# Performance work log

Hardware: AMD Instinct MI355X
Metric: run time of the kernel (lower is better)

## Reference

```python
import jax, jax.numpy as jnp
import numpy as np

B, T, D = 4, 2048, 1024
H, DH = 16, 64
GH = H * DH  # == D here
SCALE = DH ** -0.5
LN_EPS = 1e-5


def setup_inputs() -> dict:
    key = jax.random.key(0)
    ks = jax.random.split(key, 8)
    x = jax.random.normal(ks[0], (B, T, D), dtype=jnp.float32)
    attn_mask = jax.random.uniform(ks[1], (T, T), dtype=jnp.float32)
    # LayerNorm params
    gamma = jnp.ones((D,), jnp.float32)
    beta = jnp.zeros((D,), jnp.float32)
    # projection weights, stored (in, out) so y = x @ W
    Wq = jax.random.normal(ks[2], (D, GH), jnp.float32) * (D ** -0.5)
    Wk = jax.random.normal(ks[3], (D, GH), jnp.float32) * (D ** -0.5)
    Wv = jax.random.normal(ks[4], (D, GH), jnp.float32) * (D ** -0.5)
    Wo = jax.random.normal(ks[5], (GH, D), jnp.float32) * (GH ** -0.5)
    bo = jnp.zeros((D,), jnp.float32)
    return {"x": x, "attn_mask": attn_mask, "gamma": gamma, "beta": beta,
            "Wq": Wq, "Wk": Wk, "Wv": Wv, "Wo": Wo, "bo": bo}


def reference(x, attn_mask, gamma, beta, Wq, Wk, Wv, Wo, bo):
    # LayerNorm over last dim
    mu = jnp.mean(x, axis=-1, keepdims=True)
    var = jnp.mean((x - mu) ** 2, axis=-1, keepdims=True)
    xn = (x - mu) * jax.lax.rsqrt(var + LN_EPS) * gamma + beta
    # QKV projections (bias=False), reshape to [B, H, T, DH]
    split = lambda y: y.reshape(B, T, H, DH).transpose(0, 2, 1, 3)
    q = split(xn @ Wq)
    k = split(xn @ Wk)
    v = split(xn @ Wv)
    # scores scaled then MULTIPLICATIVELY masked (post-scale)
    scores = jnp.einsum('bhqd,bhkd->bhqk', q, k) * SCALE
    scores = scores * attn_mask  # broadcast [T,T] over [B,H,T,T]
    probs = jax.nn.softmax(scores, axis=-1)  # dropout p=0 -> identity
    av = jnp.einsum('bhqk,bhkd->bhqd', probs, v)
    av = av.transpose(0, 2, 1, 3).reshape(B, T, GH)
    return av @ Wo + bo
```

## Files before the change

### kernel.cpp

```cpp
#include <hip/hip_runtime.h>

typedef unsigned short u16;
typedef unsigned int u32;
typedef __bf16 bf16x8 __attribute__((ext_vector_type(8)));
typedef float f32x4 __attribute__((ext_vector_type(4)));

#define AS1 __attribute__((address_space(1)))
#define AS3 __attribute__((address_space(3)))

#define SWZB(x) ((x) ^ ((((x) >> 7) & 7) << 4))

__device__ __forceinline__ float bf2f(u16 u) {
    union { u32 i; float f; } v; v.i = ((u32)u) << 16; return v.f;
}
__device__ __forceinline__ u16 f2bf(float f) {
    union { float f; u32 i; } v; v.f = f;
    u32 i = v.i;
    u32 r = (i + 0x7fffu + ((i >> 16) & 1u)) >> 16;
    return (u16)r;
}
__device__ __forceinline__ float blo(u32 u) {
    union { u32 i; float f; } v; v.i = u << 16; return v.f;
}
__device__ __forceinline__ float bhi(u32 u) {
    union { u32 i; float f; } v; v.i = u & 0xFFFF0000u; return v.f;
}
__device__ __forceinline__ u32 cvtpk_bf16(float lo, float hi) {
    u32 r;
    asm("v_cvt_pk_bf16_f32 %0, %1, %2" : "=v"(r) : "v"(lo), "v"(hi));
    return r;
}
__device__ __forceinline__ float fexp2(float x) {
    float r;
    asm("v_exp_f32 %0, %1" : "=v"(r) : "v"(x));
    return r;
}
__device__ __forceinline__ void gload_lds16(const u16* src, u16* dst) {
    __builtin_amdgcn_global_load_lds((const AS1 void*)src, (AS3 void*)dst, 16, 0, 0);
}

__global__ __launch_bounds__(256) void transposeW(const float* __restrict__ Wq,
                                                  const float* __restrict__ Wk,
                                                  const float* __restrict__ Wv,
                                                  const float* __restrict__ Wo,
                                                  u16* __restrict__ WT,
                                                  u16* __restrict__ WoT) {
    __shared__ u16 t[64][65];
    int z = blockIdx.z;
    const float* in = (z == 0) ? Wq : (z == 1) ? Wk : (z == 2) ? Wv : Wo;
    u16* out = (z < 3) ? WT + (size_t)z * 1024 * 1024 : WoT;
    float scale = (z == 0) ? 0.18033688f : 1.0f;
    int c = threadIdx.x & 63, r0 = threadIdx.x >> 6;
    int ib = blockIdx.y * 64, jb = blockIdx.x * 64;
    #pragma unroll
    for (int r = r0; r < 64; r += 4)
        t[r][c] = f2bf(in[(size_t)(ib + r) * 1024 + jb + c] * scale);
    __syncthreads();
    #pragma unroll
    for (int r = r0; r < 64; r += 4) out[(size_t)(jb + r) * 1024 + ib + c] = t[c][r];
}

__global__ __launch_bounds__(256) void maskprep(const float* __restrict__ in,
                                                u16* __restrict__ out) {
    int i = blockIdx.x * 256 + threadIdx.x;
    float4 v = *(const float4*)&in[(size_t)i * 4];
    ushort4 o;
    o.x = f2bf(v.x); o.y = f2bf(v.y); o.z = f2bf(v.z); o.w = f2bf(v.w);
    *(ushort4*)&out[(size_t)i * 4] = o;
}

__global__ __launch_bounds__(256) void ln_kernel(const float* __restrict__ x,
                                                 const float* __restrict__ g,
                                                 const float* __restrict__ bb,
                                                 u16* __restrict__ xn) {
    int row = blockIdx.x;
    int tid = threadIdx.x;
    const float* xr = x + (size_t)row * 1024;
    float4 v = *(const float4*)&xr[tid * 4];
    float f0 = v.x, f1 = v.y, f2 = v.z, f3 = v.w;
    float s = f0 + f1 + f2 + f3;
    float sq = f0 * f0 + f1 * f1 + f2 * f2 + f3 * f3;
    #pragma unroll
    for (int m = 1; m < 64; m <<= 1) { s += __shfl_xor(s, m, 64); sq += __shfl_xor(sq, m, 64); }
    __shared__ float red[8];
    int wid = tid >> 6, lane = tid & 63;
    if (lane == 0) { red[wid] = s; red[4 + wid] = sq; }
    __syncthreads();
    s = red[0] + red[1] + red[2] + red[3];
    sq = red[4] + red[5] + red[6] + red[7];
    float mu = s * (1.f / 1024.f);
    float var = sq * (1.f / 1024.f) - mu * mu;
    float rs = rsqrtf(var + 1e-5f);
    float4 gv = *(const float4*)&g[tid * 4];
    float4 bv = *(const float4*)&bb[tid * 4];
    ushort4 o;
    o.x = f2bf((f0 - mu) * rs * gv.x + bv.x);
    o.y = f2bf((f1 - mu) * rs * gv.y + bv.y);
    o.z = f2bf((f2 - mu) * rs * gv.z + bv.z);
    o.w = f2bf((f3 - mu) * rs * gv.w + bv.w);
    *(ushort4*)&xn[(size_t)row * 1024 + tid * 4] = o;
}

__global__ __launch_bounds__(256) void gemm_bt(const u16* __restrict__ A,
                                               const u16* __restrict__ BT,
                                               u16* __restrict__ C16,
                                               float* __restrict__ C32,
                                               const float* __restrict__ bias,
                                               int K, int ldc, int ext, int nbx,
                                               u16* __restrict__ vTout) {
    __shared__ __align__(16) u16 lA[128 * 32];
    __shared__ __align__(16) u16 lB[128 * 32];
    int bid = blockIdx.x;
    int xcd = bid & 7, loc = bid >> 3;
    int npx = nbx >> 3;
    int n0 = (xcd * npx + loc % npx) * 128;
    int m0 = (loc / npx) * 128;
    int tid = threadIdx.x, lane = tid & 63, wid = tid >> 6;
    int wr = wid >> 1, wc = wid & 1;
    int l4 = lane >> 4, l15 = lane & 15;

    f32x4 acc[4][4] = {};
    int NT = K >> 5;

    auto stage = [&](int kt) {
        int k0 = kt << 5;
        #pragma unroll
        for (int i = 0; i < 2; ++i) {
            int j = wid * 2 + i;
            int row = j * 16 + (lane >> 2);
            int ch = (lane & 3) * 8;
            gload_lds16(A + (size_t)(m0 + row) * K + k0 + ch, &lA[j * 512]);
            gload_lds16(BT + (size_t)(n0 + row) * K + k0 + ch, &lB[j * 512]);
        }
    };
    stage(0);
    for (int kt = 0; kt < NT; ++kt) {
        __syncthreads();
        bf16x8 af[4], bfr[4];
        #pragma unroll
        for (int i = 0; i < 4; ++i) {
            af[i]  = *(const bf16x8*)&lA[(wr * 64 + i * 16 + l15) * 32 + l4 * 8];
            bfr[i] = *(const bf16x8*)&lB[(wc * 64 + i * 16 + l15) * 32 + l4 * 8];
        }
        __syncthreads();
        if (kt + 1 < NT) stage(kt + 1);
        #pragma unroll
        for (int i = 0; i < 4; ++i)
            #pragma unroll
            for (int j = 0; j < 4; ++j)
                acc[i][j] = __builtin_amdgcn_mfma_f32_16x16x32_bf16(af[i], bfr[j], acc[i][j], 0, 0, 0);
    }
    bool vblk = (vTout != nullptr) && (n0 >= 2048);
    #pragma unroll
    for (int j = 0; j < 4; ++j) {
        int col = n0 + wc * 64 + j * 16 + l15;
        if (vblk) {
            int hd = col - 2048;
            #pragma unroll
            for (int i = 0; i < 4; ++i) {
                int trow = m0 + wr * 64 + i * 16 + l4 * 4;
                int bidx = trow >> 11, t = trow & 2047;
                ushort4 pk;
                pk.x = f2bf(acc[i][j][0]);
                pk.y = f2bf(acc[i][j][1]);
                pk.z = f2bf(acc[i][j][2]);
                pk.w = f2bf(acc[i][j][3]);
                *(ushort4*)&vTout[(size_t)(bidx * 1024 + hd) * 2048 + t] = pk;
            }
        } else {
            float bv = ext ? bias[col] : 0.f;
            #pragma unroll
            for (int i = 0; i < 4; ++i) {
                #pragma unroll
                for (int r = 0; r < 4; ++r) {
                    int row = m0 + wr * 64 + i * 16 + l4 * 4 + r;
                    float val = acc[i][j][r] + bv;
                    if (ext) C32[(size_t)row * ldc + col] = val;
                    else     C16[(size_t)row * ldc + col] = f2bf(val);
                }
            }
        }
    }
}

__global__ __launch_bounds__(256) void attn_kernel(const u16* __restrict__ qkv,
                                                   const u16* __restrict__ vT,
                                                   const u16* __restrict__ maskb,
                                                   u16* __restrict__ av) {
    __shared__ __align__(16) u16 lK[2][64 * 64];
    __shared__ __align__(16) u16 lV[2][64 * 64];
    int qt = blockIdx.x, bh = blockIdx.y;
    int b = bh >> 4, h = bh & 15;
    int tid = threadIdx.x, lane = tid & 63, wid = tid >> 6;
    int l4 = lane >> 4, l15 = lane & 15;
    int qw = qt * 128 + wid * 32;

    const u16* qb0 = qkv + (size_t)(b * 2048 + qw + l15) * 2048 + h * 64;
    const u16* qb1 = qb0 + (size_t)16 * 2048;
    bf16x8 qf00 = *(const bf16x8*)&qb0[l4 * 8];
    bf16x8 qf01 = *(const bf16x8*)&qb0[32 + l4 * 8];
    bf16x8 qf10 = *(const bf16x8*)&qb1[l4 * 8];
    bf16x8 qf11 = *(const bf16x8*)&qb1[32 + l4 * 8];
    const u16* mrow0 = maskb + (size_t)(qw + l15) * 2048 + 8 * l4;
    const u16* mrow1 = mrow0 + (size_t)16 * 2048;

    f32x4 o0[4] = {}, o1[4] = {};
    float lsum0 = 0.f, lsum1 = 0.f;

    int c0 = tid, c1 = 256 + tid;
    auto pmap = [](int g) {
        return (g & 32) + 4 * ((g >> 3) & 3) + (g & 3) + ((g & 4) << 2);
    };
    int kd0 = SWZB(pmap(c0 >> 3) * 128 + (c0 & 7) * 16);
    int kd1 = SWZB(pmap(c1 >> 3) * 128 + (c1 & 7) * 16);
    int vd0 = SWZB((c0 >> 3) * 128 + (c0 & 7) * 16);
    int vd1 = SWZB((c1 >> 3) * 128 + (c1 & 7) * 16);
    const u16* ksrc0 = qkv + (size_t)(b * 2048 + (c0 >> 3)) * 2048 + 1024 + h * 64 + (c0 & 7) * 8;
    const u16* ksrc1 = qkv + (size_t)(b * 2048 + (c1 >> 3)) * 2048 + 1024 + h * 64 + (c1 & 7) * 8;
    const u16* vsrc0 = vT + (size_t)(bh * 64 + (c0 >> 3)) * 2048 + (c0 & 7) * 8;
    const u16* vsrc1 = vT + (size_t)(bh * 64 + (c1 >> 3)) * 2048 + (c1 & 7) * 8;

    auto loadKV = [&](int t, bf16x8& K0, bf16x8& K1, bf16x8& V0, bf16x8& V1) {
        size_t ko = (size_t)t * (64 * 2048);
        int vo = t * 64;
        K0 = *(const bf16x8*)(ksrc0 + ko);
        K1 = *(const bf16x8*)(ksrc1 + ko);
        V0 = *(const bf16x8*)(vsrc0 + vo);
        V1 = *(const bf16x8*)(vsrc1 + vo);
    };

    union PU { u32 u[4]; bf16x8 v; };

    auto body = [&](int t, int pbuf,
                    bf16x8& nK0, bf16x8& nK1, bf16x8& nV0, bf16x8& nV1,
                    bf16x8& fK0, bf16x8& fK1, bf16x8& fV0, bf16x8& fV1) {
        int k0 = t * 64;
        uint4 mua0 = *(const uint4*)(mrow0 + k0);
        uint4 mub0 = *(const uint4*)(mrow0 + k0 + 32);
        uint4 mua1 = *(const uint4*)(mrow1 + k0);
        uint4 mub1 = *(const uint4*)(mrow1 + k0 + 32);
        f32x4 mm0[4], mm1[4];
        mm0[0] = f32x4{blo(mua0.x), bhi(mua0.x), blo(mua0.y), bhi(mua0.y)};
        mm0[1] = f32x4{blo(mua0.z), bhi(mua0.z), blo(mua0.w), bhi(mua0.w)};
        mm0[2] = f32x4{blo(mub0.x), bhi(mub0.x), blo(mub0.y), bhi(mub0.y)};
        mm0[3] = f32x4{blo(mub0.z), bhi(mub0.z), blo(mub0.w), bhi(mub0.w)};
        mm1[0] = f32x4{blo(mua1.x), bhi(mua1.x), blo(mua1.y), bhi(mua1.y)};
        mm1[1] = f32x4{blo(mua1.z), bhi(mua1.z), blo(mua1.w), bhi(mua1.w)};
        mm1[2] = f32x4{blo(mub1.x), bhi(mub1.x), blo(mub1.y), bhi(mub1.y)};
        mm1[3] = f32x4{blo(mub1.z), bhi(mub1.z), blo(mub1.w), bhi(mub1.w)};
        const char* Kb = (const char*)lK[pbuf];
        f32x4 s0[4] = {}, s1[4] = {};
        __builtin_amdgcn_s_setprio(1);
        #pragma unroll
        for (int fj = 0; fj < 4; ++fj) {
            bf16x8 kf0 = *(const bf16x8*)(Kb + SWZB((fj * 16 + l15) * 128 + l4 * 16));
            bf16x8 kf1 = *(const bf16x8*)(Kb + SWZB((fj * 16 + l15) * 128 + 64 + l4 * 16));
            s0[fj] = __builtin_amdgcn_mfma_f32_16x16x32_bf16(kf0, qf00, s0[fj], 0, 0, 0);
            s0[fj] = __builtin_amdgcn_mfma_f32_16x16x32_bf16(kf1, qf01, s0[fj], 0, 0, 0);
            s1[fj] = __builtin_amdgcn_mfma_f32_16x16x32_bf16(kf0, qf10, s1[fj], 0, 0, 0);
            s1[fj] = __builtin_amdgcn_mfma_f32_16x16x32_bf16(kf1, qf11, s1[fj], 0, 0, 0);
        }
        __builtin_amdgcn_s_setprio(0);
        PU pa0[2], pa1[2];
        #pragma unroll
        for (int fj = 0; fj < 4; ++fj) {
            float p0 = fexp2(s0[fj][0] * mm0[fj][0]);
            float p1 = fexp2(s0[fj][1] * mm0[fj][1]);
            float p2 = fexp2(s0[fj][2] * mm0[fj][2]);
            float p3 = fexp2(s0[fj][3] * mm0[fj][3]);
            lsum0 += (p0 + p1) + (p2 + p3);
            int ks = fj >> 1, hf = (fj & 1) * 2;
            pa0[ks].u[hf]     = cvtpk_bf16(p0, p1);
            pa0[ks].u[hf + 1] = cvtpk_bf16(p2, p3);
        }
        #pragma unroll
        for (int fj = 0; fj < 4; ++fj) {
            float p0 = fexp2(s1[fj][0] * mm1[fj][0]);
            float p1 = fexp2(s1[fj][1] * mm1[fj][1]);
            float p2 = fexp2(s1[fj][2] * mm1[fj][2]);
            float p3 = fexp2(s1[fj][3] * mm1[fj][3]);
            lsum1 += (p0 + p1) + (p2 + p3);
            int ks = fj >> 1, hf = (fj & 1) * 2;
            pa1[ks].u[hf]     = cvtpk_bf16(p0, p1);
            pa1[ks].u[hf + 1] = cvtpk_bf16(p2, p3);
        }
        if (t + 1 < 32) {
            char* Kn = (char*)lK[pbuf ^ 1];
            char* Vn = (char*)lV[pbuf ^ 1];
            *(bf16x8*)(Kn + kd0) = nK0;
            *(bf16x8*)(Kn + kd1) = nK1;
            *(bf16x8*)(Vn + vd0) = nV0;
            *(bf16x8*)(Vn + vd1) = nV1;
        }
        if (t + 2 < 32) loadKV(t + 2, fK0, fK1, fV0, fV1);
        const char* Vb = (const char*)lV[pbuf];
        __builtin_amdgcn_s_setprio(1);
        #pragma unroll
        for (int ks = 0; ks < 2; ++ks) {
            #pragma unroll
            for (int fj = 0; fj < 4; ++fj) {
                bf16x8 vf = *(const bf16x8*)(Vb + SWZB((fj * 16 + l15) * 128 + ks * 64 + l4 * 16));
                o0[fj] = __builtin_amdgcn_mfma_f32_16x16x32_bf16(pa0[ks].v, vf, o0[fj], 0, 0, 0);
                o1[fj] = __builtin_amdgcn_mfma_f32_16x16x32_bf16(pa1[ks].v, vf, o1[fj], 0, 0, 0);
            }
        }
        __builtin_amdgcn_s_setprio(0);
        __syncthreads();
    };

    bf16x8 ka0, ka1, va0, va1, kb0, kb1, vb0, vb1;
    loadKV(0, ka0, ka1, va0, va1);
    *(bf16x8*)((char*)lK[0] + kd0) = ka0;
    *(bf16x8*)((char*)lK[0] + kd1) = ka1;
    *(bf16x8*)((char*)lV[0] + vd0) = va0;
    *(bf16x8*)((char*)lV[0] + vd1) = va1;
    loadKV(1, kb0, kb1, vb0, vb1);
    __syncthreads();
    for (int t = 0; t < 32; t += 2) {
        body(t,     0, kb0, kb1, vb0, vb1, ka0, ka1, va0, va1);
        body(t + 1, 1, ka0, ka1, va0, va1, kb0, kb1, vb0, vb1);
    }

    lsum0 += __shfl_xor(lsum0, 16, 64);
    lsum0 += __shfl_xor(lsum0, 32, 64);
    lsum1 += __shfl_xor(lsum1, 16, 64);
    lsum1 += __shfl_xor(lsum1, 32, 64);
    float den0[4], den1[4];
    #pragma unroll
    for (int r = 0; r < 4; ++r) {
        den0[r] = __shfl(lsum0, l4 * 4 + r, 64);
        den1[r] = __shfl(lsum1, l4 * 4 + r, 64);
    }
    #pragma unroll
    for (int fj = 0; fj < 4; ++fj) {
        #pragma unroll
        for (int r = 0; r < 4; ++r) {
            int col = h * 64 + fj * 16 + l15;
            av[(size_t)(b * 2048 + qw + l4 * 4 + r) * 1024 + col]      = f2bf(o0[fj][r] / den0[r]);
            av[(size_t)(b * 2048 + qw + 16 + l4 * 4 + r) * 1024 + col] = f2bf(o1[fj][r] / den1[r]);
        }
    }
}

extern "C" void kernel_launch(void* const* d_in, const int* in_sizes, int n_in,
                              void* d_out, int out_size, void* d_ws, size_t ws_size,
                              hipStream_t stream) {
    (void)in_sizes; (void)n_in; (void)out_size; (void)ws_size;
    const float* x     = (const float*)d_in[0];
    const float* mask  = (const float*)d_in[1];
    const float* gamma = (const float*)d_in[2];
    const float* beta  = (const float*)d_in[3];
    const float* Wq    = (const float*)d_in[4];
    const float* Wk    = (const float*)d_in[5];
    const float* Wv    = (const float*)d_in[6];
    const float* Wo    = (const float*)d_in[7];
    const float* bo    = (const float*)d_in[8];

    char* ws = (char*)d_ws;
    u16* xn    = (u16*)(ws);
    u16* WT    = (u16*)(ws + 16777216);
    u16* WoT   = (u16*)(ws + 23068672);
    u16* qkvb  = (u16*)(ws + 25165824);
    u16* vT    = (u16*)(ws + 58720256);
    u16* maskb = (u16*)(ws + 75497472);
    u16* av = xn;

    dim3 tb(256);
    transposeW<<<dim3(16, 16, 4), tb, 0, stream>>>(Wq, Wk, Wv, Wo, WT, WoT);
    maskprep<<<4096, tb, 0, stream>>>(mask, maskb);
    ln_kernel<<<8192, tb, 0, stream>>>(x, gamma, beta, xn);
    gemm_bt<<<24 * 64, tb, 0, stream>>>(xn, WT, qkvb, nullptr, nullptr, 1024, 2048, 0, 24, vT);
    attn_kernel<<<dim3(16, 64), tb, 0, stream>>>(qkvb, vT, maskb, av);
    gemm_bt<<<8 * 64, tb, 0, stream>>>(av, WoT, nullptr, (float*)d_out, bo, 1024, 1024, 1, 8, nullptr);
}
```

Before: 243.0 us.

## Stage K/V tiles with direct global-to-LDS loads instead of register staging

Replaces register-staged K/V prefetch (global load into VGPRs, then ds_write into swizzled LDS) with direct global-to-LDS loads. To keep the swizzled and permuted LDS layout, the source addresses are inverted from each thread's linear LDS slot. Prefetch depth drops from two tiles ahead to one, and the body is a plain loop. This frees registers and LDS-write instructions, but exposes more load latency and relies on gload_lds16 being defined and completing before the existing barrier.

```diff
diff --git a/kernel.cpp b/kernel.cpp
--- a/kernel.cpp
+++ b/kernel.cpp
@@ -208,32 +208,34 @@
     float lsum0 = 0.f, lsum1 = 0.f;
 
     int c0 = tid, c1 = 256 + tid;
-    auto pmap = [](int g) {
-        return (g & 32) + 4 * ((g >> 3) & 3) + (g & 3) + ((g & 4) << 2);
+    auto pinv = [](int p) {
+        return (p & 35) | ((p & 8) << 1) | ((p & 4) << 1) | ((p & 16) >> 2);
     };
-    int kd0 = SWZB(pmap(c0 >> 3) * 128 + (c0 & 7) * 16);
-    int kd1 = SWZB(pmap(c1 >> 3) * 128 + (c1 & 7) * 16);
-    int vd0 = SWZB((c0 >> 3) * 128 + (c0 & 7) * 16);
-    int vd1 = SWZB((c1 >> 3) * 128 + (c1 & 7) * 16);
-    const u16* ksrc0 = qkv + (size_t)(b * 2048 + (c0 >> 3)) * 2048 + 1024 + h * 64 + (c0 & 7) * 8;
-    const u16* ksrc1 = qkv + (size_t)(b * 2048 + (c1 >> 3)) * 2048 + 1024 + h * 64 + (c1 & 7) * 8;
-    const u16* vsrc0 = vT + (size_t)(bh * 64 + (c0 >> 3)) * 2048 + (c0 & 7) * 8;
-    const u16* vsrc1 = vT + (size_t)(bh * 64 + (c1 >> 3)) * 2048 + (c1 & 7) * 8;
-
-    auto loadKV = [&](int t, bf16x8& K0, bf16x8& K1, bf16x8& V0, bf16x8& V1) {
+    int u0 = SWZB(c0 * 16), u1 = SWZB(c1 * 16);
+    int kr0 = pinv(u0 >> 7), kr1 = pinv(u1 >> 7);
+    int vr0 = u0 >> 7,       vr1 = u1 >> 7;
+    int ch0 = (u0 >> 4) & 7, ch1 = (u1 >> 4) & 7;
+    const u16* kap0 = qkv + (size_t)(b * 2048 + kr0) * 2048 + 1024 + h * 64 + ch0 * 8;
+    const u16* kap1 = qkv + (size_t)(b * 2048 + kr1) * 2048 + 1024 + h * 64 + ch1 * 8;
+    const u16* vap0 = vT + (size_t)(bh * 64 + vr0) * 2048 + ch0 * 8;
+    const u16* vap1 = vT + (size_t)(bh * 64 + vr1) * 2048 + ch1 * 8;
+
+    auto stage = [&](int t, int buf) {
         size_t ko = (size_t)t * (64 * 2048);
         int vo = t * 64;
-        K0 = *(const bf16x8*)(ksrc0 + ko);
-        K1 = *(const bf16x8*)(ksrc1 + ko);
-        V0 = *(const bf16x8*)(vsrc0 + vo);
-        V1 = *(const bf16x8*)(vsrc1 + vo);
+        gload_lds16(kap0 + ko, &lK[buf][wid * 512]);
+        gload_lds16(kap1 + ko, &lK[buf][2048 + wid * 512]);
+        gload_lds16(vap0 + vo, &lV[buf][wid * 512]);
+        gload_lds16(vap1 + vo, &lV[buf][2048 + wid * 512]);
     };
 
     union PU { u32 u[4]; bf16x8 v; };
 
-    auto body = [&](int t, int pbuf,
-                    bf16x8& nK0, bf16x8& nK1, bf16x8& nV0, bf16x8& nV1,
-                    bf16x8& fK0, bf16x8& fK1, bf16x8& fV0, bf16x8& fV1) {
+    stage(0, 0);
+    __syncthreads();
+    for (int t = 0; t < 32; ++t) {
+        int pbuf = t & 1;
+        if (t + 1 < 32) stage(t + 1, pbuf ^ 1);
         int k0 = t * 64;
         uint4 mua0 = *(const uint4*)(mrow0 + k0);
         uint4 mub0 = *(const uint4*)(mrow0 + k0 + 32);
@@ -284,15 +286,6 @@
             pa1[ks].u[hf]     = cvtpk_bf16(p0, p1);
             pa1[ks].u[hf + 1] = cvtpk_bf16(p2, p3);
         }
-        if (t + 1 < 32) {
-            char* Kn = (char*)lK[pbuf ^ 1];
-            char* Vn = (char*)lV[pbuf ^ 1];
-            *(bf16x8*)(Kn + kd0) = nK0;
-            *(bf16x8*)(Kn + kd1) = nK1;
-            *(bf16x8*)(Vn + vd0) = nV0;
-            *(bf16x8*)(Vn + vd1) = nV1;
-        }
-        if (t + 2 < 32) loadKV(t + 2, fK0, fK1, fV0, fV1);
         const char* Vb = (const char*)lV[pbuf];
         __builtin_amdgcn_s_setprio(1);
         #pragma unroll
@@ -306,19 +299,6 @@
         }
         __builtin_amdgcn_s_setprio(0);
         __syncthreads();
-    };
-
-    bf16x8 ka0, ka1, va0, va1, kb0, kb1, vb0, vb1;
-    loadKV(0, ka0, ka1, va0, va1);
-    *(bf16x8*)((char*)lK[0] + kd0) = ka0;
-    *(bf16x8*)((char*)lK[0] + kd1) = ka1;
-    *(bf16x8*)((char*)lV[0] + vd0) = va0;
-    *(bf16x8*)((char*)lV[0] + vd1) = va1;
-    loadKV(1, kb0, kb1, vb0, vb1);
-    __syncthreads();
-    for (int t = 0; t < 32; t += 2) {
-        body(t,     0, kb0, kb1, vb0, vb1, ka0, ka1, va0, va1);
-        body(t + 1, 1, ka0, ka1, va0, va1, kb0, kb1, vb0, vb1);
     }
 
     lsum0 += __shfl_xor(lsum0, 16, 64);
```

Result: slower. 249.7 us (+2.7%).
